# Performance work log

Measured on AMD Instinct MI355X. Metric: run time of the kernel, lower is better.

## Reference

```python
import jax, jax.numpy as jnp
import numpy as np

HEADS = 8
DIM_HEAD = 32
SCALE = DIM_HEAD ** -0.5
EPS = 1e-5


def _layernorm_gamma(x, gamma):
    # GammaLayerNorm: zero-mean/unit-var over last dim, learnable gamma, no bias
    mu = jnp.mean(x, axis=-1, keepdims=True)
    var = jnp.var(x, axis=-1, keepdims=True)
    return (x - mu) * jax.lax.rsqrt(var + EPS) * gamma


def setup_inputs() -> dict:
    key = jax.random.key(0)
    k1, k2, k3 = jax.random.split(key, 3)
    B, N, D = 8, 16384, 256
    hidden = HEADS * DIM_HEAD  # 256
    x = jax.random.normal(k1, (B, N, D), dtype=jnp.float32)
    Wqkv = jax.random.normal(k2, (D, 3 * hidden), dtype=jnp.float32) * (D ** -0.5)
    Wout = jax.random.normal(k3, (hidden, D), dtype=jnp.float32) * (hidden ** -0.5)
    gamma = jnp.ones((D,), dtype=jnp.float32)
    return {"x": x, "Wqkv": Wqkv, "Wout": Wout, "gamma": gamma}


def reference(x, Wqkv, Wout, gamma):
    B, N, D = x.shape
    qkv = x @ Wqkv  # [B, N, 3*hidden]
    q, k, v = jnp.split(qkv, 3, axis=-1)

    def to_heads(t):  # b n (h d) -> b h n d
        return t.reshape(B, N, HEADS, DIM_HEAD).transpose(0, 2, 1, 3)

    q, k, v = map(to_heads, (q, k, v))
    q = jax.nn.softmax(q, axis=-1) * SCALE  # softmax over feature dim d
    k = jax.nn.softmax(k, axis=2)           # softmax over token dim n
    context = jnp.einsum('bhnd,bhne->bhde', k, v)  # [B,H,d,e] small kv state
    out = jnp.einsum('bhde,bhnd->bhne', context, q)  # [B,H,N,e]
    out = out.transpose(0, 2, 1, 3).reshape(B, N, HEADS * DIM_HEAD)
    out = out @ Wout
    return _layernorm_gamma(out, gamma)
```

## Files before the change

kernel.cpp:

```cpp
#include <hip/hip_runtime.h>
#include <hip/hip_bf16.h>

typedef __attribute__((ext_vector_type(8))) short short8;
typedef __attribute__((ext_vector_type(4))) float f32x4;

constexpr int SEQ = 16384, BATCH = 8, DIN = 256, NQKV = 768;
constexpr float SCALE = 0.17677669529663687f;
constexpr float EPS = 1e-5f;

__device__ __forceinline__ unsigned short f2bf(float f){
  __hip_bfloat16 h = __float2bfloat16(f);
  unsigned short u; __builtin_memcpy(&u, &h, 2); return u;
}
__device__ __forceinline__ float bf2f(unsigned short h){
  return __uint_as_float(((unsigned int)h) << 16);
}
__device__ __forceinline__ void gload_lds16(const void* g, void* l){
  __builtin_amdgcn_global_load_lds(
    (const __attribute__((address_space(1))) unsigned int*)g,
    (__attribute__((address_space(3))) unsigned int*)l, 16, 0, 0);
}

__global__ void k_wt(const float* __restrict__ W, unsigned short* __restrict__ WT){
  int id = blockIdx.x * 256 + threadIdx.x;
  int k = id / NQKV, n = id % NQKV;
  WT[n * DIN + k] = f2bf(W[id]);
}

__global__ __launch_bounds__(256) void k_qkv(const float* __restrict__ X,
                                             const unsigned short* __restrict__ WT,
                                             unsigned short* __restrict__ Q,
                                             float* __restrict__ ctxp,
                                             float* __restrict__ sumwp){
  __shared__ unsigned short Bs[2][32 * 256];
  __shared__ unsigned short WVs[2][32][136];
  __shared__ float sumLds[256];
  const int blk = blockIdx.x;
  const size_t m0 = (size_t)blk * 128;
  const int tid = threadIdx.x, wave = tid >> 6, lane = tid & 63;
  const int lg = lane >> 4, li = lane & 15;
  sumLds[tid] = 0.f;

  auto panelN0 = [](int p){
    return (p < 16) ? (((p & 1) ? 512 : 256) + (p >> 1) * 32) : (p - 16) * 32;
  };
  auto stageB = [&](int buf, int n0){
    #pragma unroll
    for (int it = 0; it < 4; it++){
      int L = (it * 256 + tid) * 16;
      int G = L ^ (((L >> 9) & 7) << 4);
      gload_lds16((const char*)WT + (size_t)(n0 + (L >> 9)) * 512 + (G & 511),
                  (char*)Bs[buf] + L);
    }
  };

  stageB(0, panelN0(0));
  short8 afrag[2][8];
  #pragma unroll
  for (int rt = 0; rt < 2; rt++){
    const float* xr = X + (m0 + wave * 32 + rt * 16 + li) * 256 + lg * 8;
    #pragma unroll
    for (int ks = 0; ks < 8; ks++){
      float4 f0 = *reinterpret_cast<const float4*>(xr + ks * 32);
      float4 f1 = *reinterpret_cast<const float4*>(xr + ks * 32 + 4);
      short8 a;
      a[0] = f2bf(f0.x); a[1] = f2bf(f0.y); a[2] = f2bf(f0.z); a[3] = f2bf(f0.w);
      a[4] = f2bf(f1.x); a[5] = f2bf(f1.y); a[6] = f2bf(f1.z); a[7] = f2bf(f1.w);
      afrag[rt][ks] = a;
    }
  }
  #pragma unroll
  for (int rt = 0; rt < 2; rt++)
    #pragma unroll
    for (int ks = 0; ks < 8; ks++)
      asm volatile("" : "+v"(afrag[rt][ks]));
  __syncthreads();

  const f32x4 zf = {0.f, 0.f, 0.f, 0.f};
  int buf = 0;
  #pragma unroll 1
  for (int p = 0; p < 24; ++p){
    if (p < 23) stageB(buf ^ 1, panelN0(p + 1));
    f32x4 acc[2][2];
    acc[0][0] = zf; acc[0][1] = zf; acc[1][0] = zf; acc[1][1] = zf;
    __builtin_amdgcn_s_setprio(1);
    #pragma unroll
    for (int ks = 0; ks < 8; ks++)
      #pragma unroll
      for (int j = 0; j < 2; j++){
        int nl = j * 16 + li;
        int L = nl * 512 + (ks * 32 + lg * 8) * 2;
        short8 bb = *reinterpret_cast<const short8*>((const char*)Bs[buf] + (L ^ ((nl & 7) << 4)));
        acc[0][j] = __builtin_amdgcn_mfma_f32_16x16x32_bf16(afrag[0][ks], bb, acc[0][j], 0, 0, 0);
        acc[1][j] = __builtin_amdgcn_mfma_f32_16x16x32_bf16(afrag[1][ks], bb, acc[1][j], 0, 0, 0);
      }
    __builtin_amdgcn_s_setprio(0);
    if (p < 16){
      int h = p >> 1;
      if (!(p & 1)){
        #pragma unroll
        for (int j = 0; j < 2; j++){
          float cs = 0.f;
          #pragma unroll
          for (int rt = 0; rt < 2; rt++){
            unsigned short h0 = f2bf(__expf(acc[rt][j][0]));
            unsigned short h1 = f2bf(__expf(acc[rt][j][1]));
            unsigned short h2 = f2bf(__expf(acc[rt][j][2]));
            unsigned short h3 = f2bf(__expf(acc[rt][j][3]));
            cs += bf2f(h0) + bf2f(h1) + bf2f(h2) + bf2f(h3);
            ushort4 pk; pk.x = h0; pk.y = h1; pk.z = h2; pk.w = h3;
            *reinterpret_cast<ushort4*>(&WVs[0][j * 16 + li][wave * 32 + rt * 16 + lg * 4]) = pk;
          }
          cs += __shfl_xor(cs, 16); cs += __shfl_xor(cs, 32);
          if (lane < 16) atomicAdd(&sumLds[h * 32 + j * 16 + li], cs);
        }
      } else {
        #pragma unroll
        for (int j = 0; j < 2; j++)
          #pragma unroll
          for (int rt = 0; rt < 2; rt++){
            ushort4 pk;
            pk.x = f2bf(acc[rt][j][0]); pk.y = f2bf(acc[rt][j][1]);
            pk.z = f2bf(acc[rt][j][2]); pk.w = f2bf(acc[rt][j][3]);
            *reinterpret_cast<ushort4*>(&WVs[1][j * 16 + li][wave * 32 + rt * 16 + lg * 4]) = pk;
          }
      }
    } else {
      int ph = p - 16;
      #pragma unroll
      for (int rt = 0; rt < 2; rt++)
        #pragma unroll
        for (int j = 0; j < 2; j++)
          #pragma unroll
          for (int r = 0; r < 4; r++)
            Q[(m0 + wave * 32 + rt * 16 + lg * 4 + r) * 256 + ph * 32 + j * 16 + li]
              = f2bf(acc[rt][j][r]);
    }
    __syncthreads();
    if (p < 16 && (p & 1)){
      int h = p >> 1;
      int dh = wave >> 1, eh = wave & 1;
      f32x4 c = zf;
      #pragma unroll
      for (int ks = 0; ks < 4; ks++){
        short8 aw = *reinterpret_cast<const short8*>(&WVs[0][dh * 16 + li][ks * 32 + lg * 8]);
        short8 bv = *reinterpret_cast<const short8*>(&WVs[1][eh * 16 + li][ks * 32 + lg * 8]);
        c = __builtin_amdgcn_mfma_f32_16x16x32_bf16(aw, bv, c, 0, 0, 0);
      }
      float* cp = ctxp + ((size_t)blk * 8 + h) * 1024;
      #pragma unroll
      for (int r = 0; r < 4; r++)
        cp[(dh * 16 + lg * 4 + r) * 32 + eh * 16 + li] = c[r];
      __syncthreads();
    }
    buf ^= 1;
  }
  sumwp[(size_t)blk * 256 + tid] = sumLds[tid];
}

__global__ __launch_bounds__(256) void k_red1(const float* __restrict__ ctxp,
                                              const float* __restrict__ sumwp,
                                              float* __restrict__ ctxr,
                                              float* __restrict__ sumr){
  int bid = blockIdx.x;
  int s = bid & 15, bh = bid >> 4;
  int b = bh >> 3, h = bh & 7;
  int t = threadIdx.x;
  float a[4] = {0.f, 0.f, 0.f, 0.f};
  #pragma unroll
  for (int k = 0; k < 8; k++){
    const float* cp = ctxp + ((size_t)(b * 128 + s * 8 + k) * 8 + h) * 1024;
    #pragma unroll
    for (int q = 0; q < 4; q++) a[q] += cp[q * 256 + t];
  }
  float* orow = ctxr + (size_t)bid * 1024;
  #pragma unroll
  for (int q = 0; q < 4; q++) orow[q * 256 + t] = a[q];
  if (t < 32){
    float sw = 0.f;
    #pragma unroll
    for (int k = 0; k < 8; k++)
      sw += sumwp[(size_t)(b * 128 + s * 8 + k) * 256 + h * 32 + t];
    sumr[(size_t)bid * 32 + t] = sw;
  }
}

__global__ __launch_bounds__(256) void k_build_m(const float* __restrict__ ctxr,
                                                 const float* __restrict__ sumr,
                                                 const float* __restrict__ Wout,
                                                 unsigned short* __restrict__ MT){
  __shared__ float ctxs[32][33];
  __shared__ float swb[32];
  int b = blockIdx.x >> 3, h = blockIdx.x & 7;
  int bh16 = (b * 8 + h) * 16;
  int t = threadIdx.x;
  int e = t & 31, dq = t >> 5;
  float a0 = 0.f, a1 = 0.f, a2 = 0.f, a3 = 0.f;
  #pragma unroll
  for (int s = 0; s < 16; s++){
    const float* cp = ctxr + (size_t)(bh16 + s) * 1024;
    a0 += cp[dq * 32 + e];         a1 += cp[(dq + 8) * 32 + e];
    a2 += cp[(dq + 16) * 32 + e];  a3 += cp[(dq + 24) * 32 + e];
  }
  if (t < 32){
    float sw = 0.f;
    #pragma unroll
    for (int s = 0; s < 16; s++) sw += sumr[(size_t)(bh16 + s) * 32 + t];
    swb[t] = sw;
  }
  __syncthreads();
  ctxs[dq][e]      = a0 / swb[dq];
  ctxs[dq + 8][e]  = a1 / swb[dq + 8];
  ctxs[dq + 16][e] = a2 / swb[dq + 16];
  ctxs[dq + 24][e] = a3 / swb[dq + 24];
  __syncthreads();
  float s[32];
  #pragma unroll
  for (int d = 0; d < 32; d++) s[d] = 0.f;
  for (int ee = 0; ee < 32; ee++){
    float wv = Wout[(size_t)(h * 32 + ee) * 256 + t];
    #pragma unroll
    for (int d = 0; d < 32; d++) s[d] += ctxs[d][ee] * wv;
  }
  unsigned short* mp = MT + (size_t)b * 65536 + (size_t)t * 256 + h * 32;
  #pragma unroll
  for (int d8 = 0; d8 < 4; d8++){
    short8 pk;
    #pragma unroll
    for (int q = 0; q < 8; q++) pk[q] = (short)f2bf(s[d8 * 8 + q]);
    *reinterpret_cast<short8*>(mp + d8 * 8) = pk;
  }
}

__global__ __launch_bounds__(256, 4) void k_out(const unsigned short* __restrict__ Qm,
                                                const unsigned short* __restrict__ MT,
                                                const float* __restrict__ gamma,
                                                float* __restrict__ out){
  __shared__ unsigned short Bs[64 * 256];
  const int blk = blockIdx.x;
  const int b = blk >> 8;
  const size_t m0 = (size_t)blk * 64;
  const int tid = threadIdx.x, wave = tid >> 6, lane = tid & 63;
  const int lg = lane >> 4, li = lane & 15;

  short8 afrag[8];
  {
    const unsigned short* qr = Qm + (m0 + wave * 16 + li) * 256 + lg * 8;
    #pragma unroll
    for (int ks = 0; ks < 8; ks++)
      afrag[ks] = *reinterpret_cast<const short8*>(qr + ks * 32);
  }
  #pragma unroll
  for (int ks = 0; ks < 8; ks++){
    float v[8];
    #pragma unroll
    for (int q = 0; q < 8; q++) v[q] = bf2f((unsigned short)afrag[ks][q]);
    float mx = v[0];
    #pragma unroll
    for (int q = 1; q < 8; q++) mx = fmaxf(mx, v[q]);
    mx = fmaxf(mx, __shfl_xor(mx, 16));
    mx = fmaxf(mx, __shfl_xor(mx, 32));
    float s = 0.f;
    #pragma unroll
    for (int q = 0; q < 8; q++){ v[q] = __expf(v[q] - mx); s += v[q]; }
    s += __shfl_xor(s, 16);
    s += __shfl_xor(s, 32);
    float iv = SCALE / s;
    #pragma unroll
    for (int q = 0; q < 8; q++) afrag[ks][q] = (short)f2bf(v[q] * iv);
  }

  const char* mtb = (const char*)MT + (size_t)b * 131072;
  f32x4 acc[4][4];
  const f32x4 zf = {0.f, 0.f, 0.f, 0.f};
  #pragma unroll
  for (int jb = 0; jb < 4; jb++)
    #pragma unroll
    for (int j = 0; j < 4; j++) acc[jb][j] = zf;

  #pragma unroll
  for (int jb = 0; jb < 4; jb++){
    if (jb) __syncthreads();
    #pragma unroll
    for (int rr = 0; rr < 8; rr++){
      int L = rr * 4096 + tid * 16;
      int G = L ^ (((L >> 9) & 7) << 4);
      gload_lds16(mtb + (size_t)jb * 32768 + G, (char*)Bs + L);
    }
    __syncthreads();
    #pragma unroll
    for (int ks = 0; ks < 8; ks++)
      #pragma unroll
      for (int j = 0; j < 4; j++){
        int n = j * 16 + li;
        int L = n * 512 + (ks * 32 + lg * 8) * 2;
        short8 bb = *reinterpret_cast<const short8*>((const char*)Bs + (L ^ ((n & 7) << 4)));
        acc[jb][j] = __builtin_amdgcn_mfma_f32_16x16x32_bf16(afrag[ks], bb, acc[jb][j], 0, 0, 0);
      }
  }

  float gam[16];
  #pragma unroll
  for (int jb = 0; jb < 4; jb++)
    #pragma unroll
    for (int j = 0; j < 4; j++) gam[jb * 4 + j] = gamma[jb * 64 + j * 16 + li];
  #pragma unroll
  for (int r = 0; r < 4; r++){
    float s = 0.f, qq = 0.f;
    #pragma unroll
    for (int jb = 0; jb < 4; jb++)
      #pragma unroll
      for (int j = 0; j < 4; j++){ float v = acc[jb][j][r]; s += v; qq += v * v; }
    #pragma unroll
    for (int mm = 1; mm < 16; mm <<= 1){ s += __shfl_xor(s, mm); qq += __shfl_xor(qq, mm); }
    float mu = s * (1.f / 256.f);
    float var = qq * (1.f / 256.f) - mu * mu;
    float inv = rsqrtf(var + EPS);
    float* op = out + (m0 + wave * 16 + lg * 4 + r) * 256;
    #pragma unroll
    for (int jb = 0; jb < 4; jb++)
      #pragma unroll
      for (int j = 0; j < 4; j++)
        op[jb * 64 + j * 16 + li] = (acc[jb][j][r] - mu) * inv * gam[jb * 4 + j];
  }
}

extern "C" void kernel_launch(void* const* d_in, const int* in_sizes, int n_in,
                              void* d_out, int out_size, void* d_ws, size_t ws_size,
                              hipStream_t stream){
  const float* x     = (const float*)d_in[0];
  const float* Wqkv  = (const float*)d_in[1];
  const float* Wout  = (const float*)d_in[2];
  const float* gamma = (const float*)d_in[3];
  float* out = (float*)d_out;

  char* ws = (char*)d_ws;
  size_t off = 0;
  unsigned short* Q   = (unsigned short*)(ws + off); off += (size_t)BATCH * SEQ * 256 * 2;
  unsigned short* WT  = (unsigned short*)(ws + off); off += (size_t)NQKV * DIN * 2;
  float* ctxp         = (float*)(ws + off);          off += (size_t)1024 * 8 * 1024 * 4;
  float* sumwp        = (float*)(ws + off);          off += (size_t)1024 * 256 * 4;
  float* ctxr         = (float*)(ws + off);          off += (size_t)1024 * 1024 * 4;
  float* sumr         = (float*)(ws + off);          off += (size_t)1024 * 32 * 4;
  unsigned short* MT  = (unsigned short*)(ws + off); off += (size_t)BATCH * 65536 * 2;

  k_wt<<<(NQKV * DIN) / 256, 256, 0, stream>>>(Wqkv, WT);
  k_qkv<<<1024, 256, 0, stream>>>(x, WT, Q, ctxp, sumwp);
  k_red1<<<1024, 256, 0, stream>>>(ctxp, sumwp, ctxr, sumr);
  k_build_m<<<64, 256, 0, stream>>>(ctxr, sumr, Wout, MT);
  k_out<<<2048, 256, 0, stream>>>(Q, MT, gamma, out);
}
```

Baseline: 178.2 us.

## Remove per-panel block barriers by computing context per wave and accumulating in LDS

The weight panels are no longer staged into double-buffered LDS with global_load_lds; each lane now reads its B fragments straight from global memory (L2-resident weights). The per-head context outer product is computed per wave on its own 32 rows, and the four partial results are combined with LDS atomicAdds into a padded ctx_lds buffer. That buffer is written out once at the end, so the per-iteration __syncthreads are gone. The cost is direct global loads on the MFMA critical path with no prefetch, plus many LDS float atomics. The s_setprio hints are also dropped.

New measurement: 336.8 us. 89.1% more time.

```diff
diff --git a/kernel.cpp b/kernel.cpp
--- a/kernel.cpp
+++ b/kernel.cpp
@@ -32,29 +32,22 @@
                                              unsigned short* __restrict__ Q,
                                              float* __restrict__ ctxp,
                                              float* __restrict__ sumwp){
-  __shared__ unsigned short Bs[2][32 * 256];
-  __shared__ unsigned short WVs[2][32][136];
+  __shared__ unsigned short Tw[4][32][34];
+  __shared__ unsigned short Tv[4][32][34];
+  __shared__ float ctx_lds[8 * 1056];
   __shared__ float sumLds[256];
   const int blk = blockIdx.x;
   const size_t m0 = (size_t)blk * 128;
   const int tid = threadIdx.x, wave = tid >> 6, lane = tid & 63;
   const int lg = lane >> 4, li = lane & 15;
+
+  for (int i = tid; i < 8448; i += 256) ctx_lds[i] = 0.f;
   sumLds[tid] = 0.f;
 
   auto panelN0 = [](int p){
     return (p < 16) ? (((p & 1) ? 512 : 256) + (p >> 1) * 32) : (p - 16) * 32;
   };
-  auto stageB = [&](int buf, int n0){
-    #pragma unroll
-    for (int it = 0; it < 4; it++){
-      int L = (it * 256 + tid) * 16;
-      int G = L ^ (((L >> 9) & 7) << 4);
-      gload_lds16((const char*)WT + (size_t)(n0 + (L >> 9)) * 512 + (G & 511),
-                  (char*)Bs[buf] + L);
-    }
-  };
-
-  stageB(0, panelN0(0));
+
   short8 afrag[2][8];
   #pragma unroll
   for (int rt = 0; rt < 2; rt++){
@@ -77,24 +70,24 @@
   __syncthreads();
 
   const f32x4 zf = {0.f, 0.f, 0.f, 0.f};
-  int buf = 0;
+  const unsigned short* wtl = WT + (size_t)li * 256 + lg * 8;
+
   #pragma unroll 1
   for (int p = 0; p < 24; ++p){
-    if (p < 23) stageB(buf ^ 1, panelN0(p + 1));
+    const int n0 = panelN0(p);
+    const unsigned short* b0p = wtl + (size_t)n0 * 256;
+    const unsigned short* b1p = b0p + 16 * 256;
     f32x4 acc[2][2];
     acc[0][0] = zf; acc[0][1] = zf; acc[1][0] = zf; acc[1][1] = zf;
-    __builtin_amdgcn_s_setprio(1);
-    #pragma unroll
-    for (int ks = 0; ks < 8; ks++)
-      #pragma unroll
-      for (int j = 0; j < 2; j++){
-        int nl = j * 16 + li;
-        int L = nl * 512 + (ks * 32 + lg * 8) * 2;
-        short8 bb = *reinterpret_cast<const short8*>((const char*)Bs[buf] + (L ^ ((nl & 7) << 4)));
-        acc[0][j] = __builtin_amdgcn_mfma_f32_16x16x32_bf16(afrag[0][ks], bb, acc[0][j], 0, 0, 0);
-        acc[1][j] = __builtin_amdgcn_mfma_f32_16x16x32_bf16(afrag[1][ks], bb, acc[1][j], 0, 0, 0);
-      }
-    __builtin_amdgcn_s_setprio(0);
+    #pragma unroll
+    for (int ks = 0; ks < 8; ks++){
+      short8 b0 = *reinterpret_cast<const short8*>(b0p + ks * 32);
+      short8 b1 = *reinterpret_cast<const short8*>(b1p + ks * 32);
+      acc[0][0] = __builtin_amdgcn_mfma_f32_16x16x32_bf16(afrag[0][ks], b0, acc[0][0], 0, 0, 0);
+      acc[1][0] = __builtin_amdgcn_mfma_f32_16x16x32_bf16(afrag[1][ks], b0, acc[1][0], 0, 0, 0);
+      acc[0][1] = __builtin_amdgcn_mfma_f32_16x16x32_bf16(afrag[0][ks], b1, acc[0][1], 0, 0, 0);
+      acc[1][1] = __builtin_amdgcn_mfma_f32_16x16x32_bf16(afrag[1][ks], b1, acc[1][1], 0, 0, 0);
+    }
     if (p < 16){
       int h = p >> 1;
       if (!(p & 1)){
@@ -109,7 +102,7 @@
             unsigned short h3 = f2bf(__expf(acc[rt][j][3]));
             cs += bf2f(h0) + bf2f(h1) + bf2f(h2) + bf2f(h3);
             ushort4 pk; pk.x = h0; pk.y = h1; pk.z = h2; pk.w = h3;
-            *reinterpret_cast<ushort4*>(&WVs[0][j * 16 + li][wave * 32 + rt * 16 + lg * 4]) = pk;
+            *reinterpret_cast<ushort4*>(&Tw[wave][j * 16 + li][rt * 16 + lg * 4]) = pk;
           }
           cs += __shfl_xor(cs, 16); cs += __shfl_xor(cs, 32);
           if (lane < 16) atomicAdd(&sumLds[h * 32 + j * 16 + li], cs);
@@ -122,7 +115,18 @@
             ushort4 pk;
             pk.x = f2bf(acc[rt][j][0]); pk.y = f2bf(acc[rt][j][1]);
             pk.z = f2bf(acc[rt][j][2]); pk.w = f2bf(acc[rt][j][3]);
-            *reinterpret_cast<ushort4*>(&WVs[1][j * 16 + li][wave * 32 + rt * 16 + lg * 4]) = pk;
+            *reinterpret_cast<ushort4*>(&Tv[wave][j * 16 + li][rt * 16 + lg * 4]) = pk;
+          }
+        #pragma unroll
+        for (int dh = 0; dh < 2; dh++)
+          #pragma unroll
+          for (int eh = 0; eh < 2; eh++){
+            short8 aw = *reinterpret_cast<const short8*>(&Tw[wave][dh * 16 + li][lg * 8]);
+            short8 bv = *reinterpret_cast<const short8*>(&Tv[wave][eh * 16 + li][lg * 8]);
+            f32x4 c = __builtin_amdgcn_mfma_f32_16x16x32_bf16(aw, bv, zf, 0, 0, 0);
+            #pragma unroll
+            for (int r = 0; r < 4; r++)
+              atomicAdd(&ctx_lds[h * 1056 + (dh * 16 + lg * 4 + r) * 33 + eh * 16 + li], c[r]);
           }
       }
     } else {
@@ -136,24 +140,11 @@
             Q[(m0 + wave * 32 + rt * 16 + lg * 4 + r) * 256 + ph * 32 + j * 16 + li]
               = f2bf(acc[rt][j][r]);
     }
-    __syncthreads();
-    if (p < 16 && (p & 1)){
-      int h = p >> 1;
-      int dh = wave >> 1, eh = wave & 1;
-      f32x4 c = zf;
-      #pragma unroll
-      for (int ks = 0; ks < 4; ks++){
-        short8 aw = *reinterpret_cast<const short8*>(&WVs[0][dh * 16 + li][ks * 32 + lg * 8]);
-        short8 bv = *reinterpret_cast<const short8*>(&WVs[1][eh * 16 + li][ks * 32 + lg * 8]);
-        c = __builtin_amdgcn_mfma_f32_16x16x32_bf16(aw, bv, c, 0, 0, 0);
-      }
-      float* cp = ctxp + ((size_t)blk * 8 + h) * 1024;
-      #pragma unroll
-      for (int r = 0; r < 4; r++)
-        cp[(dh * 16 + lg * 4 + r) * 32 + eh * 16 + li] = c[r];
-      __syncthreads();
-    }
-    buf ^= 1;
+  }
+  __syncthreads();
+  for (int i = tid; i < 8192; i += 256){
+    int h = i >> 10, de = i & 1023;
+    ctxp[(size_t)blk * 8192 + i] = ctx_lds[h * 1056 + (de >> 5) * 33 + (de & 31)];
   }
   sumwp[(size_t)blk * 256 + tid] = sumLds[tid];
 }
```
